# Kernel tuning notes

Measured on AMD Instinct MI355X. Metric: run time of the kernel, lower is better.

Reference implementation:

```python
import jax, jax.numpy as jnp
import numpy as np

B, T, D, H, K, V = 2, 2048, 2048, 16, 128, 128


def _l2norm(x, eps=1e-12):
    # F.normalize(p=2, dim=-1)
    n = jnp.sqrt(jnp.sum(x * x, axis=-1, keepdims=True))
    return x / jnp.maximum(n, eps)


def setup_inputs() -> dict:
    key = jax.random.key(0)
    ks = jax.random.split(key, 7)
    s = D ** -0.5
    return {
        "x": jax.random.normal(ks[0], (B, T, D), jnp.float32),
        "Wq": jax.random.normal(ks[1], (H * K, D), jnp.float32) * s,
        "Wk": jax.random.normal(ks[2], (H * K, D), jnp.float32) * s,
        "Wv": jax.random.normal(ks[3], (H * V, D), jnp.float32) * s,
        "Wa": jax.random.normal(ks[4], (H, D), jnp.float32) * s,
        "ba": jnp.zeros((H,), jnp.float32),
        "Wb": jax.random.normal(ks[5], (H, D), jnp.float32) * s,
        "bb": jnp.zeros((H,), jnp.float32),
    }


def _forward(x, Wq, Wk, Wv, Wa, ba, Wb, bb):
    Bq, Tq, _ = x.shape
    # projections (nn.Linear: y = x @ W.T)
    q = _l2norm(jnp.einsum('btd,od->bto', x, Wq).reshape(Bq, Tq, H, K))
    k = _l2norm(jnp.einsum('btd,od->bto', x, Wk).reshape(Bq, Tq, H, K))
    v = jnp.einsum('btd,od->bto', x, Wv).reshape(Bq, Tq, H, V)
    alpha = jax.nn.sigmoid(jnp.einsum('btd,hd->bth', x, Wa) + ba)          # [B,T,H] decay in (0,1)
    beta = jax.nn.softplus(jnp.einsum('btd,hd->bth', x, Wb) + bb) * K ** (-0.5)

    # gated delta rule recurrence over time (vectorized over B,H):
    #   S_t = a_t * S_{t-1} (I - b_t k_t k_t^T) + b_t v_t k_t^T ;  o_t = S_t q_t
    def step(S, inp):
        q_t, k_t, v_t, a_t, b_t = inp  # [B,H,K],[B,H,K],[B,H,V],[B,H],[B,H]
        Sd = S * a_t[..., None, None]                              # decay  [B,H,V,K]
        pred = jnp.einsum('bhvk,bhk->bhv', Sd, k_t)                # S k
        u = b_t[..., None] * (v_t - pred)                          # delta update [B,H,V]
        S_new = Sd + u[..., None] * k_t[:, :, None, :]             # rank-1 write
        o_t = jnp.einsum('bhvk,bhk->bhv', S_new, q_t)
        return S_new, o_t

    S0 = jnp.zeros((Bq, H, V, K), x.dtype)
    xs = (q.transpose(1, 0, 2, 3), k.transpose(1, 0, 2, 3),
          v.transpose(1, 0, 2, 3), alpha.transpose(1, 0, 2), beta.transpose(1, 0, 2))
    _, o = jax.lax.scan(step, S0, xs)
    return o.transpose(1, 0, 2, 3)  # [B,T,H,V]


def reference(x, Wq, Wk, Wv, Wa, ba, Wb, bb):
    return _forward(x, Wq, Wk, Wv, Wa, ba, Wb, bb)
```

## Files before the change

kernel.cpp:

```cpp
#include <hip/hip_runtime.h>
#include <math.h>

#define BB 2
#define TT 2048
#define DD 2048
#define HH 16
#define KK 128

typedef _Float16 h4 __attribute__((ext_vector_type(4)));
typedef _Float16 v8h __attribute__((ext_vector_type(8)));
typedef float v4f __attribute__((ext_vector_type(4)));
typedef float v2f __attribute__((ext_vector_type(2)));

__global__ __launch_bounds__(256) void gemm_nt3(const float* __restrict__ A,
                                                const float* __restrict__ W0,
                                                const float* __restrict__ W1,
                                                const float* __restrict__ W2,
                                                float* __restrict__ Cbase,
                                                int M, int N, int Kd) {
  __shared__ float As[8][128];
  __shared__ float Bs[8][128];
  const int z = blockIdx.z;
  const float* W = (z == 0) ? W0 : (z == 1) ? W1 : W2;
  float* C = Cbase + (size_t)z * M * N;
  const int tid = threadIdx.x;
  const int bm = blockIdx.y * 128;
  const int bn = blockIdx.x * 128;
  const int lrow = tid >> 1;
  const int lcol = (tid & 1) * 4;
  const int rm = (tid >> 4) * 8;
  const int rn = (tid & 15) * 8;
  const float* Ap = A + (size_t)(bm + lrow) * Kd + lcol;
  const float* Wp = W + (size_t)(bn + lrow) * Kd + lcol;
  float acc[8][8];
#pragma unroll
  for (int i = 0; i < 8; i++)
#pragma unroll
    for (int j = 0; j < 8; j++) acc[i][j] = 0.f;
  float4 av = *(const float4*)Ap;
  float4 wv = *(const float4*)Wp;
  for (int d0 = 0; d0 < Kd; d0 += 8) {
    __syncthreads();
    As[lcol + 0][lrow] = av.x; As[lcol + 1][lrow] = av.y;
    As[lcol + 2][lrow] = av.z; As[lcol + 3][lrow] = av.w;
    Bs[lcol + 0][lrow] = wv.x; Bs[lcol + 1][lrow] = wv.y;
    Bs[lcol + 2][lrow] = wv.z; Bs[lcol + 3][lrow] = wv.w;
    __syncthreads();
    if (d0 + 8 < Kd) {
      av = *(const float4*)(Ap + d0 + 8);
      wv = *(const float4*)(Wp + d0 + 8);
    }
#pragma unroll
    for (int kk = 0; kk < 8; kk++) {
      const float4 a0 = *(const float4*)&As[kk][rm];
      const float4 a1 = *(const float4*)&As[kk][rm + 4];
      const float4 b0 = *(const float4*)&Bs[kk][rn];
      const float4 b1 = *(const float4*)&Bs[kk][rn + 4];
      const float ar[8] = {a0.x, a0.y, a0.z, a0.w, a1.x, a1.y, a1.z, a1.w};
      const float br[8] = {b0.x, b0.y, b0.z, b0.w, b1.x, b1.y, b1.z, b1.w};
#pragma unroll
      for (int i = 0; i < 8; i++)
#pragma unroll
        for (int j = 0; j < 8; j++) acc[i][j] = fmaf(ar[i], br[j], acc[i][j]);
    }
  }
#pragma unroll
  for (int i = 0; i < 8; i++) {
    float* cp = C + (size_t)(bm + rm + i) * N + bn + rn;
    float4 c0 = {acc[i][0], acc[i][1], acc[i][2], acc[i][3]};
    float4 c1 = {acc[i][4], acc[i][5], acc[i][6], acc[i][7]};
    *(float4*)cp = c0;
    *(float4*)(cp + 4) = c1;
  }
}

__global__ __launch_bounds__(256) void convert_f16(
    const float* __restrict__ x, const float* __restrict__ Wq,
    const float* __restrict__ Wk, const float* __restrict__ Wv,
    _Float16* __restrict__ xh, _Float16* __restrict__ xl,
    _Float16* __restrict__ Wf) {
  const size_t N4X = (size_t)BB * TT * DD / 4;
  const size_t N4W = (size_t)(HH * KK) * DD / 4;
  const size_t i = (size_t)blockIdx.x * 256 + threadIdx.x;
  if (i < N4X) {
    const float4 v = ((const float4*)x)[i];
    h4 hi, lo;
    hi.x = (_Float16)v.x; hi.y = (_Float16)v.y;
    hi.z = (_Float16)v.z; hi.w = (_Float16)v.w;
    lo.x = (_Float16)(v.x - (float)hi.x);
    lo.y = (_Float16)(v.y - (float)hi.y);
    lo.z = (_Float16)(v.z - (float)hi.z);
    lo.w = (_Float16)(v.w - (float)hi.w);
    ((h4*)xh)[i] = hi;
    ((h4*)xl)[i] = lo;
  } else {
    const size_t j = i - N4X;
    const float* Ws = (j < N4W) ? Wq : (j < 2 * N4W) ? Wk : Wv;
    const size_t jj = (j < N4W) ? j : (j < 2 * N4W) ? (j - N4W) : (j - 2 * N4W);
    const float4 v = ((const float4*)Ws)[jj];
    h4 hi;
    hi.x = (_Float16)v.x; hi.y = (_Float16)v.y;
    hi.z = (_Float16)v.z; hi.w = (_Float16)v.w;
    ((h4*)Wf)[j] = hi;
  }
}

#define GLDS(gp, lp)                                              \
  __builtin_amdgcn_global_load_lds(                               \
      (const __attribute__((address_space(1))) void*)(gp),        \
      (__attribute__((address_space(3))) void*)(lp), 16, 0, 0)
#define GLDS4(gp, lp)                                             \
  __builtin_amdgcn_global_load_lds(                               \
      (const __attribute__((address_space(1))) void*)(gp),        \
      (__attribute__((address_space(3))) void*)(lp), 4, 0, 0)

__global__ __launch_bounds__(256) void gemm_mfma(
    const _Float16* __restrict__ xh, const _Float16* __restrict__ xl,
    const _Float16* __restrict__ Wf, float* __restrict__ Cbase) {
  __shared__ float4 lraw[1536];
  _Float16* Ah = (_Float16*)lraw;
  _Float16* Al = Ah + 4096;
  _Float16* Bs = Al + 4096;

  const int z = blockIdx.z;
  const _Float16* W = Wf + (size_t)z * DD * (HH * KK);
  float* C = Cbase + (size_t)z * (BB * TT) * (HH * KK);

  const int tid = threadIdx.x;
  const int w = tid >> 6;
  const int lane = tid & 63;
  const int bm = blockIdx.y * 128;
  const int bn = blockIdx.x * 128;
  const int wm = (w & 1) * 64;
  const int wn = (w >> 1) * 64;
  const int m16 = lane & 15;
  const int quad = lane >> 4;

  const _Float16* gAh = xh + (size_t)(bm + (tid >> 2)) * DD + (tid & 3) * 8;
  const _Float16* gAl = xl + (size_t)(bm + (tid >> 2)) * DD + (tid & 3) * 8;
  const _Float16* gB = W + (size_t)(bn + (tid >> 2)) * DD + (tid & 3) * 8;
  const int lb = w * 512;

  v4f acc[4][4];
#pragma unroll
  for (int i = 0; i < 4; i++)
#pragma unroll
    for (int j = 0; j < 4; j++) acc[i][j] = (v4f){0.f, 0.f, 0.f, 0.f};

  for (int d0 = 0; d0 < DD; d0 += 32) {
    GLDS(gAh + d0, Ah + lb);
    GLDS(gAh + d0 + 64 * DD, Ah + 2048 + lb);
    GLDS(gAl + d0, Al + lb);
    GLDS(gAl + d0 + 64 * DD, Al + 2048 + lb);
    GLDS(gB + d0, Bs + lb);
    GLDS(gB + d0 + 64 * DD, Bs + 2048 + lb);
    __syncthreads();
    v8h ah[4], al[4], bw[4];
#pragma unroll
    for (int i = 0; i < 4; i++) {
      ah[i] = *(const v8h*)&Ah[(wm + i * 16 + m16) * 32 + quad * 8];
      al[i] = *(const v8h*)&Al[(wm + i * 16 + m16) * 32 + quad * 8];
      bw[i] = *(const v8h*)&Bs[(wn + i * 16 + m16) * 32 + quad * 8];
    }
#pragma unroll
    for (int mi = 0; mi < 4; mi++)
#pragma unroll
      for (int ni = 0; ni < 4; ni++) {
        acc[mi][ni] = __builtin_amdgcn_mfma_f32_16x16x32_f16(ah[mi], bw[ni],
                                                             acc[mi][ni], 0, 0, 0);
        acc[mi][ni] = __builtin_amdgcn_mfma_f32_16x16x32_f16(al[mi], bw[ni],
                                                             acc[mi][ni], 0, 0, 0);
      }
    __syncthreads();
  }
#pragma unroll
  for (int mi = 0; mi < 4; mi++) {
#pragma unroll
    for (int r = 0; r < 4; r++) {
      float* cp =
          C + (size_t)(bm + wm + mi * 16 + quad * 4 + r) * (HH * KK) + bn + wn + m16;
#pragma unroll
      for (int ni = 0; ni < 4; ni++) cp[ni * 16] = acc[mi][ni][r];
    }
  }
}

__global__ __launch_bounds__(64) void ab_proj(const float* __restrict__ x,
                                              const float* __restrict__ Wa,
                                              const float* __restrict__ ba,
                                              const float* __restrict__ Wb,
                                              const float* __restrict__ bb,
                                              float* __restrict__ abq) {
  const int row = blockIdx.x;
  const int g = blockIdx.y;
  const int h0 = (g & 1) * 8;
  const bool isA = (g < 2);
  const float* W = isA ? Wa : Wb;
  const int lane = threadIdx.x;
  const float* xr = x + (size_t)row * DD;
  float acc[8];
#pragma unroll
  for (int j = 0; j < 8; j++) acc[j] = 0.f;
  for (int d = lane; d < DD; d += 64) {
    const float xv = xr[d];
#pragma unroll
    for (int j = 0; j < 8; j++)
      acc[j] = fmaf(xv, W[(size_t)(h0 + j) * DD + d], acc[j]);
  }
#pragma unroll
  for (int j = 0; j < 8; j++) {
#pragma unroll
    for (int off = 32; off > 0; off >>= 1) acc[j] += __shfl_xor(acc[j], off, 64);
  }
  if (lane == 0) {
    if (isA) {
#pragma unroll
      for (int j = 0; j < 8; j++) {
        const float z = acc[j] + ba[h0 + j];
        abq[((size_t)row * HH + h0 + j) * 4 + 0] = 1.0f / (1.0f + expf(-z));
      }
    } else {
#pragma unroll
      for (int j = 0; j < 8; j++) {
        const float z = acc[j] + bb[h0 + j];
        const float sp = (z > 20.f) ? z : log1pf(expf(z));
        abq[((size_t)row * HH + h0 + j) * 4 + 1] = sp * 0.08838834764831845f;
      }
    }
  }
}

__global__ __launch_bounds__(256) void norm_qk(float* __restrict__ q,
                                               float* __restrict__ k,
                                               float* __restrict__ abq) {
  const int vec = blockIdx.x * 4 + (threadIdx.x >> 6);
  const int l = threadIdx.x & 63;
  float* qp = q + (size_t)vec * 128;
  float* kp = k + (size_t)vec * 128;
  float q0 = qp[l], q1 = qp[l + 64];
  float k0 = kp[l], k1 = kp[l + 64];
  float sq = q0 * q0 + q1 * q1;
  float sk = k0 * k0 + k1 * k1;
#pragma unroll
  for (int off = 32; off > 0; off >>= 1) {
    sq += __shfl_xor(sq, off, 64);
    sk += __shfl_xor(sk, off, 64);
  }
  const float iq = 1.0f / fmaxf(sqrtf(sq), 1e-12f);
  const float ik = 1.0f / fmaxf(sqrtf(sk), 1e-12f);
  q0 *= iq; q1 *= iq; k0 *= ik; k1 *= ik;
  qp[l] = q0; qp[l + 64] = q1;
  kp[l] = k0; kp[l + 64] = k1;
  float pq = q0 * k0 + q1 * k1;
#pragma unroll
  for (int off = 32; off > 0; off >>= 1) pq += __shfl_xor(pq, off, 64);
  if (l == 0) abq[(size_t)vec * 4 + 2] = pq;
}

#define DPP_ADD(x, ctrl)                                                     \
  ((x) + __int_as_float(__builtin_amdgcn_update_dpp(                         \
             0, __float_as_int(x), (ctrl), 0xF, 0xF, true)))

#define WSTEPS 8
#define NWIN (TT / WSTEPS)
#define VB 32768
#define ABB 34816
#define V2F(p) (*(const v2f*)&(p))

struct Slot {
  float4 kA, kB, qA, qB, ab;
  float vv;
};

__global__ __launch_bounds__(256) void scan_kernel(const float* __restrict__ q,
                                                   const float* __restrict__ k,
                                                   const float* __restrict__ v,
                                                   const float* __restrict__ abq,
                                                   float* __restrict__ o) {
  __shared__ __attribute__((aligned(16))) char lds[35328];
  const int bid = blockIdx.x;
  const int bh = bid & 31;
  const int s = bid >> 5;
  const int h = bh & 15;
  const int b = bh >> 4;
  const int tid = threadIdx.x;
  const int w = tid >> 6;
  const int lane = tid & 63;
  const int rg = lane >> 4;
  const int g = lane & 15;
  const int rowloc = w * 4 + rg;
  const int vrow = s * 16 + rowloc;

  float* ob = o + (size_t)b * TT * 2048 + (size_t)h * KK + vrow;

  auto stage = [&](int Wst) {
    const int t0 = Wst * WSTEPS;
    const int slot = Wst & 3;
#pragma unroll
    for (int i = 0; i < 3; i++) {
      const int id = w * 3 + i;
      if (id < 8) {
        const int t = t0 + id;
        const size_t vecbase = ((size_t)(b * TT + t) * HH + h) * 128;
        const float* src = (lane < 32) ? (k + vecbase + lane * 4)
                                       : (q + vecbase + (size_t)(lane - 32) * 4);
        GLDS(src, lds + slot * 8192 + id * 1024);
      } else if (id < 10) {
        const int t4 = t0 + (id - 8) * 4;
        const float* src = v + (size_t)(b * TT + t4 + (lane >> 4)) * 2048 +
                           h * 128 + s * 16 + (lane & 15);
        GLDS4(src, lds + VB + slot * 512 + (id - 8) * 256);
      } else {
        if (lane < 8) {
          const float* src =
              abq + ((size_t)(b * TT + t0 + lane) * HH + h) * 4;
          GLDS(src, lds + ABB + slot * 128);
        }
      }
    }
  };

#define LOAD_SLOT(S_, t_)                                                   \
  {                                                                         \
    const int _m = (t_) & 31;                                               \
    S_.kA = *(const float4*)(lds + _m * 1024 + g * 32);                     \
    S_.kB = *(const float4*)(lds + _m * 1024 + g * 32 + 16);                \
    S_.qA = *(const float4*)(lds + _m * 1024 + 512 + g * 32);               \
    S_.qB = *(const float4*)(lds + _m * 1024 + 512 + g * 32 + 16);          \
    S_.vv = *(const float*)(lds + VB + _m * 64 + rowloc * 4);               \
    S_.ab = *(const float4*)(lds + ABB + _m * 16);                          \
  }

#define STEP(S_, t_)                                                        \
  {                                                                         \
    const v2f k0 = V2F(S_.kA.x), k1 = V2F(S_.kA.z);                         \
    const v2f k2 = V2F(S_.kB.x), k3 = V2F(S_.kB.z);                         \
    const v2f q0 = V2F(S_.qA.x), q1 = V2F(S_.qA.z);                         \
    const v2f q2 = V2F(S_.qB.x), q3 = V2F(S_.qB.z);                         \
    v2f aK = __builtin_elementwise_fma(                                     \
        k0, Sv0,                                                            \
        __builtin_elementwise_fma(                                          \
            k1, Sv1, __builtin_elementwise_fma(k2, Sv2, k3 * Sv3)));        \
    v2f aQ = __builtin_elementwise_fma(                                     \
        q0, Sv0,                                                            \
        __builtin_elementwise_fma(                                          \
            q1, Sv1, __builtin_elementwise_fma(q2, Sv2, q3 * Sv3)));        \
    float dk = aK.x + aK.y, dq = aQ.x + aQ.y;                               \
    dk = DPP_ADD(dk, 0xB1);  dq = DPP_ADD(dq, 0xB1);                        \
    dk = DPP_ADD(dk, 0x4E);  dq = DPP_ADD(dq, 0x4E);                        \
    dk = DPP_ADD(dk, 0x141); dq = DPP_ADD(dq, 0x141);                       \
    dk = DPP_ADD(dk, 0x140); dq = DPP_ADD(dq, 0x140);                       \
    const float a_ = S_.ab.x, b_ = S_.ab.y, kqd = S_.ab.z;                  \
    const float u = b_ * (S_.vv - a_ * dk);                                 \
    const float oo = fmaf(a_, dq, u * kqd);                                 \
    const v2f a2 = {a_, a_}, u2 = {u, u};                                   \
    Sv0 = __builtin_elementwise_fma(a2, Sv0, u2 * k0);                      \
    Sv1 = __builtin_elementwise_fma(a2, Sv1, u2 * k1);                      \
    Sv2 = __builtin_elementwise_fma(a2, Sv2, u2 * k2);                      \
    Sv3 = __builtin_elementwise_fma(a2, Sv3, u2 * k3);                      \
    if (g == 0) ob[(size_t)(t_) * 2048] = oo;                               \
  }

  stage(0);
  stage(1);
  __builtin_amdgcn_s_waitcnt(0x0F70);
  __builtin_amdgcn_s_barrier();

  Slot slA, slB;
  LOAD_SLOT(slA, 0);
  LOAD_SLOT(slB, 1);

  v2f Sv0 = {0.f, 0.f}, Sv1 = {0.f, 0.f}, Sv2 = {0.f, 0.f}, Sv3 = {0.f, 0.f};

  for (int W = 0; W < NWIN; W++) {
    if (W >= 1) {
      __builtin_amdgcn_s_waitcnt(0x0F78);
      __builtin_amdgcn_s_barrier();
    }
    if (W + 2 < NWIN) stage(W + 2);
    const int t0 = W * WSTEPS;
#pragma unroll
    for (int j = 0; j < WSTEPS; j += 2) {
      const int t = t0 + j;
      STEP(slA, t);
      {
        const int tp = (t + 2 < TT) ? t + 2 : t;
        LOAD_SLOT(slA, tp);
      }
      __builtin_amdgcn_sched_barrier(0);
      STEP(slB, t + 1);
      {
        const int tp = (t + 3 < TT) ? t + 3 : t;
        LOAD_SLOT(slB, tp);
      }
      __builtin_amdgcn_sched_barrier(0);
    }
  }
}

extern "C" void kernel_launch(void* const* d_in, const int* in_sizes, int n_in,
                              void* d_out, int out_size, void* d_ws,
                              size_t ws_size, hipStream_t stream) {
  const float* x = (const float*)d_in[0];
  const float* Wq = (const float*)d_in[1];
  const float* Wk = (const float*)d_in[2];
  const float* Wv = (const float*)d_in[3];
  const float* Wa = (const float*)d_in[4];
  const float* ba = (const float*)d_in[5];
  const float* Wb = (const float*)d_in[6];
  const float* bb = (const float*)d_in[7];
  float* out = (float*)d_out;
  float* ws = (float*)d_ws;

  const size_t PROJ = (size_t)BB * TT * HH * KK;
  const size_t NABQ = (size_t)BB * TT * HH * 4;
  float* qw = ws;
  float* kw = ws + PROJ;
  float* vw = ws + 2 * PROJ;
  float* abq = ws + 3 * PROJ;
  _Float16* xh = (_Float16*)(abq + NABQ);
  _Float16* xl = xh + (size_t)BB * TT * DD;
  _Float16* Wf = xl + (size_t)BB * TT * DD;
  const size_t NEED = (3 * PROJ + NABQ) * 4 +
                      ((size_t)BB * TT * DD * 2 + 3 * (size_t)(HH * KK) * DD) * 2;

  const int M = BB * TT;
  const int N = HH * KK;
  if (ws_size >= NEED) {
    const int cgrid = (int)(((size_t)BB * TT * DD / 4 + 3 * (size_t)N * DD / 4) / 256);
    convert_f16<<<cgrid, 256, 0, stream>>>(x, Wq, Wk, Wv, xh, xl, Wf);
    gemm_mfma<<<dim3(N / 128, M / 128, 3), 256, 0, stream>>>(xh, xl, Wf, qw);
  } else {
    gemm_nt3<<<dim3(N / 128, M / 128, 3), 256, 0, stream>>>(x, Wq, Wk, Wv, qw,
                                                            M, N, DD);
  }
  ab_proj<<<dim3(M, 4), 64, 0, stream>>>(x, Wa, ba, Wb, bb, abq);
  norm_qk<<<(BB * TT * HH) / 4, 256, 0, stream>>>(qw, kw, abq);
  scan_kernel<<<BB * HH * 8, 256, 0, stream>>>(qw, kw, vw, abq, out);
}
```

Baseline: 814.8 us.

## Pack normalized q/k as fp16 and halve scan kernel LDS traffic

The normalization kernel now writes the L2-normalized k and q vectors as interleaved fp16 into a reused workspace buffer, and the scan kernel stages and reads these half-precision vectors. This halves the global and LDS bytes for k/q per step and shrinks shared memory. The v staging layout is also reorganized so each row's eight timesteps are contiguous. In exchange, the recurrence uses fp16-rounded k and q, which costs accuracy, and each step adds per-element conversions back to fp32.

```diff
diff --git a/kernel.cpp b/kernel.cpp
--- a/kernel.cpp
+++ b/kernel.cpp
@@ -10,7 +10,6 @@
 typedef _Float16 h4 __attribute__((ext_vector_type(4)));
 typedef _Float16 v8h __attribute__((ext_vector_type(8)));
 typedef float v4f __attribute__((ext_vector_type(4)));
-typedef float v2f __attribute__((ext_vector_type(2)));
 
 __global__ __launch_bounds__(256) void gemm_nt3(const float* __restrict__ A,
                                                 const float* __restrict__ W0,
@@ -230,13 +229,14 @@
   }
 }
 
-__global__ __launch_bounds__(256) void norm_qk(float* __restrict__ q,
-                                               float* __restrict__ k,
-                                               float* __restrict__ abq) {
+__global__ __launch_bounds__(256) void norm_pack(const float* __restrict__ q,
+                                                 const float* __restrict__ k,
+                                                 _Float16* __restrict__ kq,
+                                                 float* __restrict__ abq) {
   const int vec = blockIdx.x * 4 + (threadIdx.x >> 6);
   const int l = threadIdx.x & 63;
-  float* qp = q + (size_t)vec * 128;
-  float* kp = k + (size_t)vec * 128;
+  const float* qp = q + (size_t)vec * 128;
+  const float* kp = k + (size_t)vec * 128;
   float q0 = qp[l], q1 = qp[l + 64];
   float k0 = kp[l], k1 = kp[l + 64];
   float sq = q0 * q0 + q1 * q1;
@@ -248,10 +248,14 @@
   }
   const float iq = 1.0f / fmaxf(sqrtf(sq), 1e-12f);
   const float ik = 1.0f / fmaxf(sqrtf(sk), 1e-12f);
-  q0 *= iq; q1 *= iq; k0 *= ik; k1 *= ik;
-  qp[l] = q0; qp[l + 64] = q1;
-  kp[l] = k0; kp[l + 64] = k1;
-  float pq = q0 * k0 + q1 * k1;
+  const _Float16 hq0 = (_Float16)(q0 * iq), hq1 = (_Float16)(q1 * iq);
+  const _Float16 hk0 = (_Float16)(k0 * ik), hk1 = (_Float16)(k1 * ik);
+  _Float16* kv = kq + (size_t)vec * 256;
+  kv[l] = hk0;
+  kv[l + 64] = hk1;
+  kv[l + 128] = hq0;
+  kv[l + 192] = hq1;
+  float pq = (float)hq0 * (float)hk0 + (float)hq1 * (float)hk1;
 #pragma unroll
   for (int off = 32; off > 0; off >>= 1) pq += __shfl_xor(pq, off, 64);
   if (l == 0) abq[(size_t)vec * 4 + 2] = pq;
@@ -263,21 +267,19 @@
 
 #define WSTEPS 8
 #define NWIN (TT / WSTEPS)
-#define VB 32768
-#define ABB 34816
-#define V2F(p) (*(const v2f*)&(p))
+#define VB 16384
+#define ABB 18432
 
 struct Slot {
-  float4 kA, kB, qA, qB, ab;
+  v8h kh, qh;
+  float4 ab;
   float vv;
 };
 
-__global__ __launch_bounds__(256) void scan_kernel(const float* __restrict__ q,
-                                                   const float* __restrict__ k,
-                                                   const float* __restrict__ v,
-                                                   const float* __restrict__ abq,
-                                                   float* __restrict__ o) {
-  __shared__ __attribute__((aligned(16))) char lds[35328];
+__global__ __launch_bounds__(256) void scan_kernel(
+    const _Float16* __restrict__ kq, const float* __restrict__ v,
+    const float* __restrict__ abq, float* __restrict__ o) {
+  __shared__ __attribute__((aligned(16))) char lds[18944];
   const int bid = blockIdx.x;
   const int bh = bid & 31;
   const int s = bid >> 5;
@@ -297,23 +299,22 @@
     const int t0 = Wst * WSTEPS;
     const int slot = Wst & 3;
 #pragma unroll
-    for (int i = 0; i < 3; i++) {
-      const int id = w * 3 + i;
-      if (id < 8) {
-        const int t = t0 + id;
-        const size_t vecbase = ((size_t)(b * TT + t) * HH + h) * 128;
-        const float* src = (lane < 32) ? (k + vecbase + lane * 4)
-                                       : (q + vecbase + (size_t)(lane - 32) * 4);
-        GLDS(src, lds + slot * 8192 + id * 1024);
-      } else if (id < 10) {
-        const int t4 = t0 + (id - 8) * 4;
-        const float* src = v + (size_t)(b * TT + t4 + (lane >> 4)) * 2048 +
-                           h * 128 + s * 16 + (lane & 15);
-        GLDS4(src, lds + VB + slot * 512 + (id - 8) * 256);
-      } else {
+    for (int i = 0; i < 2; i++) {
+      const int id = w * 2 + i;
+      if (id < 4) {
+        const int t = t0 + 2 * id + (lane >> 5);
+        const _Float16* src =
+            kq + ((size_t)(b * TT + t) * HH + h) * 256 + (size_t)(lane & 31) * 8;
+        GLDS(src, lds + slot * 4096 + id * 1024);
+      } else if (id < 6) {
+        const int n = id - 4;
+        const float* src = v +
+                           (size_t)(b * TT + t0 + (lane & 7)) * 2048 + h * 128 +
+                           s * 16 + 8 * n + (lane >> 3);
+        GLDS4(src, lds + VB + slot * 512 + n * 256);
+      } else if (id == 6) {
         if (lane < 8) {
-          const float* src =
-              abq + ((size_t)(b * TT + t0 + lane) * HH + h) * 4;
+          const float* src = abq + ((size_t)(b * TT + t0 + lane) * HH + h) * 4;
           GLDS(src, lds + ABB + slot * 128);
         }
       }
@@ -322,30 +323,32 @@
 
 #define LOAD_SLOT(S_, t_)                                                   \
   {                                                                         \
-    const int _m = (t_) & 31;                                               \
-    S_.kA = *(const float4*)(lds + _m * 1024 + g * 32);                     \
-    S_.kB = *(const float4*)(lds + _m * 1024 + g * 32 + 16);                \
-    S_.qA = *(const float4*)(lds + _m * 1024 + 512 + g * 32);               \
-    S_.qB = *(const float4*)(lds + _m * 1024 + 512 + g * 32 + 16);          \
-    S_.vv = *(const float*)(lds + VB + _m * 64 + rowloc * 4);               \
-    S_.ab = *(const float4*)(lds + ABB + _m * 16);                          \
+    const int _sl = ((t_) >> 3) & 3;                                        \
+    const int _j = (t_) & 7;                                                \
+    const char* _sb = lds + _sl * 4096 + _j * 512;                          \
+    S_.kh = *(const v8h*)(_sb + g * 16);                                    \
+    S_.qh = *(const v8h*)(_sb + 256 + g * 16);                              \
+    S_.vv = *(const float*)(lds + VB + _sl * 512 + rowloc * 32 + _j * 4);   \
+    S_.ab = *(const float4*)(lds + ABB + _sl * 128 + _j * 16);              \
   }
 
 #define STEP(S_, t_)                                                        \
   {                                                                         \
-    const v2f k0 = V2F(S_.kA.x), k1 = V2F(S_.kA.z);                         \
-    const v2f k2 = V2F(S_.kB.x), k3 = V2F(S_.kB.z);                         \
-    const v2f q0 = V2F(S_.qA.x), q1 = V2F(S_.qA.z);                         \
-    const v2f q2 = V2F(S_.qB.x), q3 = V2F(S_.qB.z);                         \
-    v2f aK = __builtin_elementwise_fma(                                     \
-        k0, Sv0,                                                            \
-        __builtin_elementwise_fma(                                          \
-            k1, Sv1, __builtin_elementwise_fma(k2, Sv2, k3 * Sv3)));        \
-    v2f aQ = __builtin_elementwise_fma(                                     \
-        q0, Sv0,                                                            \
-        __builtin_elementwise_fma(                                          \
-            q1, Sv1, __builtin_elementwise_fma(q2, Sv2, q3 * Sv3)));        \
-    float dk = aK.x + aK.y, dq = aQ.x + aQ.y;                               \
+    const v8h kh = S_.kh;                                                   \
+    const v8h qh = S_.qh;                                                   \
+    float dkA = fmaf((float)kh[1], S1, (float)kh[0] * S0);                  \
+    dkA = fmaf((float)kh[2], S2, dkA);                                      \
+    dkA = fmaf((float)kh[3], S3, dkA);                                      \
+    float dkB = fmaf((float)kh[5], S5, (float)kh[4] * S4);                  \
+    dkB = fmaf((float)kh[6], S6, dkB);                                      \
+    dkB = fmaf((float)kh[7], S7, dkB);                                      \
+    float dqA = fmaf((float)qh[1], S1, (float)qh[0] * S0);                  \
+    dqA = fmaf((float)qh[2], S2, dqA);                                      \
+    dqA = fmaf((float)qh[3], S3, dqA);                                      \
+    float dqB = fmaf((float)qh[5], S5, (float)qh[4] * S4);                  \
+    dqB = fmaf((float)qh[6], S6, dqB);                                      \
+    dqB = fmaf((float)qh[7], S7, dqB);                                      \
+    float dk = dkA + dkB, dq = dqA + dqB;                                   \
     dk = DPP_ADD(dk, 0xB1);  dq = DPP_ADD(dq, 0xB1);                        \
     dk = DPP_ADD(dk, 0x4E);  dq = DPP_ADD(dq, 0x4E);                        \
     dk = DPP_ADD(dk, 0x141); dq = DPP_ADD(dq, 0x141);                       \
@@ -353,11 +356,14 @@
     const float a_ = S_.ab.x, b_ = S_.ab.y, kqd = S_.ab.z;                  \
     const float u = b_ * (S_.vv - a_ * dk);                                 \
     const float oo = fmaf(a_, dq, u * kqd);                                 \
-    const v2f a2 = {a_, a_}, u2 = {u, u};                                   \
-    Sv0 = __builtin_elementwise_fma(a2, Sv0, u2 * k0);                      \
-    Sv1 = __builtin_elementwise_fma(a2, Sv1, u2 * k1);                      \
-    Sv2 = __builtin_elementwise_fma(a2, Sv2, u2 * k2);                      \
-    Sv3 = __builtin_elementwise_fma(a2, Sv3, u2 * k3);                      \
+    S0 = fmaf(a_, S0, u * (float)kh[0]);                                    \
+    S1 = fmaf(a_, S1, u * (float)kh[1]);                                    \
+    S2 = fmaf(a_, S2, u * (float)kh[2]);                                    \
+    S3 = fmaf(a_, S3, u * (float)kh[3]);                                    \
+    S4 = fmaf(a_, S4, u * (float)kh[4]);                                    \
+    S5 = fmaf(a_, S5, u * (float)kh[5]);                                    \
+    S6 = fmaf(a_, S6, u * (float)kh[6]);                                    \
+    S7 = fmaf(a_, S7, u * (float)kh[7]);                                    \
     if (g == 0) ob[(size_t)(t_) * 2048] = oo;                               \
   }
 
@@ -370,7 +376,8 @@
   LOAD_SLOT(slA, 0);
   LOAD_SLOT(slB, 1);
 
-  v2f Sv0 = {0.f, 0.f}, Sv1 = {0.f, 0.f}, Sv2 = {0.f, 0.f}, Sv3 = {0.f, 0.f};
+  float S0 = 0.f, S1 = 0.f, S2 = 0.f, S3 = 0.f;
+  float S4 = 0.f, S5 = 0.f, S6 = 0.f, S7 = 0.f;
 
   for (int W = 0; W < NWIN; W++) {
     if (W >= 1) {
@@ -426,15 +433,18 @@
 
   const int M = BB * TT;
   const int N = HH * KK;
+  _Float16* kqf16;
   if (ws_size >= NEED) {
     const int cgrid = (int)(((size_t)BB * TT * DD / 4 + 3 * (size_t)N * DD / 4) / 256);
     convert_f16<<<cgrid, 256, 0, stream>>>(x, Wq, Wk, Wv, xh, xl, Wf);
     gemm_mfma<<<dim3(N / 128, M / 128, 3), 256, 0, stream>>>(xh, xl, Wf, qw);
+    kqf16 = xh;
   } else {
     gemm_nt3<<<dim3(N / 128, M / 128, 3), 256, 0, stream>>>(x, Wq, Wk, Wv, qw,
                                                             M, N, DD);
+    kqf16 = (_Float16*)(abq + NABQ);
   }
   ab_proj<<<dim3(M, 4), 64, 0, stream>>>(x, Wa, ba, Wb, bb, abq);
-  norm_qk<<<(BB * TT * HH) / 4, 256, 0, stream>>>(qw, kw, abq);
-  scan_kernel<<<BB * HH * 8, 256, 0, stream>>>(qw, kw, vw, abq, out);
-}
+  norm_pack<<<(BB * TT * HH) / 4, 256, 0, stream>>>(qw, kw, kqf16, abq);
+  scan_kernel<<<BB * HH * 8, 256, 0, stream>>>(kqf16, vw, abq, out);
+}
```

After: 835.3 us. 2.5% more time.
